# Performance work log

Hardware: AMD Instinct MI355X
Metric: run time of the kernel (lower is better)

The kernel has to match this reference:

```python
import jax, jax.numpy as jnp
import numpy as np

NUM_GROUPS = 16
EPS = 1e-6


def setup_inputs() -> dict:
    key = jax.random.key(0)
    ks = jax.random.split(key, 6)
    b, c, t, h, w = 2, 256, 4, 32, 32
    x = jax.random.normal(ks[0], (b, c, t, h, w), dtype=jnp.float32)
    scale = 0.02
    return {
        "x": x,
        "gamma": jnp.ones((c,), jnp.float32),
        "beta": jnp.zeros((c,), jnp.float32),
        "wq": jax.random.normal(ks[1], (c, c), jnp.float32) * scale,
        "bq": jnp.zeros((c,), jnp.float32),
        "wk": jax.random.normal(ks[2], (c, c), jnp.float32) * scale,
        "bk": jnp.zeros((c,), jnp.float32),
        "wv": jax.random.normal(ks[3], (c, c), jnp.float32) * scale,
        "bv": jnp.zeros((c,), jnp.float32),
        "wp": jax.random.normal(ks[4], (c, c), jnp.float32) * scale,
        "bp": jnp.zeros((c,), jnp.float32),
    }


def _group_norm(x, gamma, beta):
    b, c, t, h, w = x.shape
    xg = x.reshape(b, NUM_GROUPS, -1)  # [b, G, (c/G)*t*h*w]
    mu = jnp.mean(xg, axis=2, keepdims=True)
    var = jnp.var(xg, axis=2, keepdims=True)
    xn = ((xg - mu) * jax.lax.rsqrt(var + EPS)).reshape(b, c, t, h, w)
    return xn * gamma[None, :, None, None, None] + beta[None, :, None, None, None]


def reference(x, gamma, beta, wq, bq, wk, bk, wv, bv, wp, bp):
    b, c, t, h, w = x.shape
    n = t * h * w
    hn = _group_norm(x, gamma, beta).reshape(b, c, n)  # [b, c, n]
    # 1x1x1 conv == channel matmul
    q = jnp.einsum("oc,bcn->bon", wq, hn) + bq[None, :, None]
    k = jnp.einsum("oc,bcn->bon", wk, hn) + bk[None, :, None]
    v = jnp.einsum("oc,bcn->bon", wv, hn) + bv[None, :, None]
    # scores[b, i, j] = sum_c q[b,c,i] k[b,c,j] / sqrt(c)
    scores = jnp.einsum("bci,bcj->bij", q, k) * (float(c) ** -0.5)
    attn = jax.nn.softmax(scores, axis=2)  # [b, n, n]
    # h_[b, c, i] = sum_j v[b,c,j] attn[b,i,j]
    ho = jnp.einsum("bcj,bij->bci", v, attn)
    out = jnp.einsum("oc,bcn->bon", wp, ho) + bp[None, :, None]
    return x + out.reshape(b, c, t, h, w)
```

## Files before the change

kernel.cpp:

```cpp
#include <hip/hip_runtime.h>
#include <hip/hip_bf16.h>

#define NB 2
#define NC 256
#define NN 4096
#define NG 16
#define GSZ (16*NN)
#define SPLIT 4
#define SCL 0.09014205f

typedef __attribute__((ext_vector_type(8))) short bf16x8;
typedef __attribute__((ext_vector_type(4))) float f32x4;
typedef __attribute__((ext_vector_type(8))) unsigned short u16x8;

static __device__ __forceinline__ unsigned short f2b(float f) {
    union { float f; unsigned u; } x; x.f = f;
    unsigned r = x.u + 0x7fffu + ((x.u >> 16) & 1u);
    return (unsigned short)(r >> 16);
}
static __device__ __forceinline__ float b2f(unsigned short u) {
    union { unsigned u; float f; } x; x.u = ((unsigned)u) << 16;
    return x.f;
}
static __device__ __forceinline__ void glds16(const void* g, void* l) {
    __builtin_amdgcn_global_load_lds(
        (const __attribute__((address_space(1))) unsigned int*)g,
        (__attribute__((address_space(3))) unsigned int*)l, 16, 0, 0);
}

__global__ void k_wcvt(const float* __restrict__ wq, const float* __restrict__ wk,
                       const float* __restrict__ wv, const float* __restrict__ wp,
                       unsigned short* __restrict__ dst) {
    int idx = (blockIdx.x * 256 + threadIdx.x) * 4;
    int which = idx >> 16, off = idx & 65535;
    const float* s = (which == 0) ? wq : (which == 1) ? wk : (which == 2) ? wv : wp;
    float4 v = *(const float4*)(s + off);
    dst[idx + 0] = f2b(v.x);
    dst[idx + 1] = f2b(v.y);
    dst[idx + 2] = f2b(v.z);
    dst[idx + 3] = f2b(v.w);
}

__global__ void k_stats(const float* __restrict__ x, float* __restrict__ stats) {
    int bg = blockIdx.x >> 3, seg = blockIdx.x & 7;
    const float4* p = (const float4*)(x + (size_t)bg * GSZ + (size_t)seg * (GSZ / 8));
    float s1 = 0.f, s2 = 0.f;
    for (int k = threadIdx.x; k < GSZ / 8 / 4; k += 256) {
        float4 v = p[k];
        s1 += v.x + v.y + v.z + v.w;
        s2 += v.x*v.x + v.y*v.y + v.z*v.z + v.w*v.w;
    }
    #pragma unroll
    for (int m = 1; m < 64; m <<= 1) { s1 += __shfl_xor(s1, m); s2 += __shfl_xor(s2, m); }
    __shared__ float r1[4], r2[4];
    int w = threadIdx.x >> 6;
    if ((threadIdx.x & 63) == 0) { r1[w] = s1; r2[w] = s2; }
    __syncthreads();
    if (threadIdx.x == 0) {
        float a = 0.f, b = 0.f;
        #pragma unroll
        for (int i = 0; i < 4; i++) { a += r1[i]; b += r2[i]; }
        atomicAdd(&stats[bg * 2], a);
        atomicAdd(&stats[bg * 2 + 1], b);
    }
}

__global__ void k_norm_t(const float* __restrict__ x, const float* __restrict__ gamma,
                         const float* __restrict__ beta, const float* __restrict__ stats,
                         unsigned short* __restrict__ hn_t) {
    __shared__ unsigned short tile[64][66];
    int n0 = blockIdx.x * 64, c0 = blockIdx.y * 64, b = blockIdx.z;
    int cc = threadIdx.x >> 2, part = threadIdx.x & 3;
    int c = c0 + cc;
    float s1 = stats[(b * NG + (c >> 4)) * 2];
    float s2 = stats[(b * NG + (c >> 4)) * 2 + 1];
    float mean = s1 * (1.f / (float)GSZ);
    float var  = s2 * (1.f / (float)GSZ) - mean * mean;
    float rstd = rsqrtf(var + 1e-6f);
    float sc = rstd * gamma[c];
    float sh = beta[c] - mean * sc;
    const float4* row = (const float4*)(x + ((size_t)b * NC + c) * NN + n0);
    #pragma unroll
    for (int q = 0; q < 4; q++) {
        int f4 = part * 4 + q;
        float4 v = row[f4];
        tile[cc][f4*4+0] = f2b(v.x * sc + sh);
        tile[cc][f4*4+1] = f2b(v.y * sc + sh);
        tile[cc][f4*4+2] = f2b(v.z * sc + sh);
        tile[cc][f4*4+3] = f2b(v.w * sc + sh);
    }
    __syncthreads();
    int nn = threadIdx.x >> 2;
    u16x8 o0, o1;
    #pragma unroll
    for (int e = 0; e < 8; e++) { o0[e] = tile[part*16 + e][nn]; o1[e] = tile[part*16 + 8 + e][nn]; }
    unsigned short* dst = hn_t + ((size_t)b * NN + n0 + nn) * NC + c0 + part * 16;
    *(u16x8*)dst = o0;
    *(u16x8*)(dst + 8) = o1;
}

__global__ __launch_bounds__(256, 2) void k_qkv(
        const unsigned short* __restrict__ hn_t, const unsigned short* __restrict__ wb,
        const float* __restrict__ bq, const float* __restrict__ bk, const float* __restrict__ bv,
        unsigned short* __restrict__ q_t, unsigned short* __restrict__ k_t,
        unsigned short* __restrict__ v_cm) {
    int i0 = blockIdx.x * 64, which = blockIdx.y, b = blockIdx.z;
    int lane = threadIdx.x & 63, w = threadIdx.x >> 6;
    const unsigned short* W = wb + which * 65536;
    const float* bias = (which == 0) ? bq : (which == 1) ? bk : bv;
    if (which < 2) {
        const unsigned short* arow =
            hn_t + ((size_t)b * NN + i0 + w * 16 + (lane & 15)) * NC + ((lane >> 4) * 8);
        f32x4 acc[16];
        #pragma unroll
        for (int t = 0; t < 16; t++) acc[t] = (f32x4){0.f, 0.f, 0.f, 0.f};
        #pragma unroll
        for (int kk = 0; kk < 8; kk++) {
            bf16x8 af = *(const bf16x8*)(arow + kk * 32);
            const unsigned short* bbase = W + (size_t)(lane & 15) * NC + kk * 32 + ((lane >> 4) * 8);
            #pragma unroll
            for (int ot = 0; ot < 16; ot++) {
                bf16x8 bf_ = *(const bf16x8*)(bbase + (size_t)ot * 16 * NC);
                acc[ot] = __builtin_amdgcn_mfma_f32_16x16x32_bf16(af, bf_, acc[ot], 0, 0, 0);
            }
        }
        unsigned short* dst = ((which == 0) ? q_t : k_t) + (size_t)b * NN * NC;
        #pragma unroll
        for (int ot = 0; ot < 16; ot++) {
            float bv_ = bias[ot * 16 + (lane & 15)];
            #pragma unroll
            for (int r = 0; r < 4; r++) {
                int i = i0 + w * 16 + (lane >> 4) * 4 + r;
                dst[(size_t)i * NC + ot * 16 + (lane & 15)] = f2b(acc[ot][r] + bv_);
            }
        }
    } else {
        f32x4 acc[4][4];
        #pragma unroll
        for (int mt = 0; mt < 4; mt++)
            #pragma unroll
            for (int nt = 0; nt < 4; nt++) acc[mt][nt] = (f32x4){0.f, 0.f, 0.f, 0.f};
        #pragma unroll
        for (int kk = 0; kk < 8; kk++) {
            bf16x8 bfr[4];
            #pragma unroll
            for (int nt = 0; nt < 4; nt++)
                bfr[nt] = *(const bf16x8*)(hn_t + ((size_t)b * NN + i0 + nt * 16 + (lane & 15)) * NC
                                           + kk * 32 + ((lane >> 4) * 8));
            #pragma unroll
            for (int mt = 0; mt < 4; mt++) {
                bf16x8 af = *(const bf16x8*)(W + (size_t)(w * 64 + mt * 16 + (lane & 15)) * NC
                                             + kk * 32 + ((lane >> 4) * 8));
                #pragma unroll
                for (int nt = 0; nt < 4; nt++)
                    acc[mt][nt] = __builtin_amdgcn_mfma_f32_16x16x32_bf16(af, bfr[nt], acc[mt][nt], 0, 0, 0);
            }
        }
        #pragma unroll
        for (int mt = 0; mt < 4; mt++) {
            #pragma unroll
            for (int r = 0; r < 4; r++) {
                int o = w * 64 + mt * 16 + (lane >> 4) * 4 + r;
                float bv_ = bias[o];
                #pragma unroll
                for (int nt = 0; nt < 4; nt++) {
                    int i = i0 + nt * 16 + (lane & 15);
                    v_cm[(size_t)b * NC * NN + (size_t)o * NN + i] = f2b(acc[mt][nt][r] + bv_);
                }
            }
        }
    }
}

__global__ __launch_bounds__(512, 2) void k_attn(
        const unsigned short* __restrict__ q_t, const unsigned short* __restrict__ k_t,
        const unsigned short* __restrict__ v_cm,
        unsigned short* __restrict__ po, float* __restrict__ ml) {
    __shared__ __attribute__((aligned(16))) unsigned short Ks[2][16384];
    __shared__ __attribute__((aligned(16))) unsigned short Vs[2][16384];
    __shared__ __attribute__((aligned(16))) unsigned short Ps[8][1024];
    int d = blockIdx.x;
    int g = d & 7, xb = d >> 3;
    int sp = g & 3, b = g >> 2;
    int i0 = xb * 128;
    int lane = threadIdx.x & 63, w = threadIdx.x >> 6;
    size_t bO = (size_t)b * NN * NC;
    bf16x8 qf[8];
    {
        const unsigned short* qrow =
            q_t + bO + (size_t)(i0 + w * 16 + (lane & 15)) * NC + ((lane >> 4) * 8);
        #pragma unroll
        for (int kk = 0; kk < 8; kk++) qf[kk] = *(const bf16x8*)(qrow + kk * 32);
    }
    int j0b = sp * 1024;
    const char* gpk[4];
    const char* gpv[4];
    {
        const char* kbase = (const char*)(k_t + bO);
        const char* vbase = (const char*)(v_cm + bO);
        #pragma unroll
        for (int r = 0; r < 4; r++) {
            int jr = r * 16 + w * 2 + (lane >> 5);
            int cb = (lane & 31) * 16;
            gpk[r] = kbase + (size_t)(j0b + jr) * 512 + (cb ^ ((jr & 7) << 4));
            int cr = r * 64 + w * 8 + (lane >> 3);
            int jb = (lane & 7) * 16;
            gpv[r] = vbase + (size_t)cr * 8192 + (size_t)j0b * 2 + (jb ^ ((cr & 7) << 4));
        }
    }
    f32x4 o[16];
    #pragma unroll
    for (int t = 0; t < 16; t++) o[t] = (f32x4){0.f, 0.f, 0.f, 0.f};
    float m[4], l[4];
    #pragma unroll
    for (int r = 0; r < 4; r++) { m[r] = -1e30f; l[r] = 0.f; }
    #pragma unroll
    for (int r = 0; r < 4; r++) {
        glds16(gpk[r], (char*)&Ks[0][0] + w * 1024 + r * 8192);
        glds16(gpv[r], (char*)&Vs[0][0] + w * 1024 + r * 8192);
    }
    __syncthreads();
    int cur = 0;
    #pragma unroll 1
    for (int t = 0; t < 16; ++t) {
        if (t < 15) {
            #pragma unroll
            for (int r = 0; r < 4; r++) { gpk[r] += 32768; gpv[r] += 128; }
            int nb = cur ^ 1;
            #pragma unroll
            for (int r = 0; r < 4; r++) {
                glds16(gpk[r], (char*)&Ks[nb][0] + w * 1024 + r * 8192);
                glds16(gpv[r], (char*)&Vs[nb][0] + w * 1024 + r * 8192);
            }
        }
        const char* KsB = (const char*)&Ks[cur][0];
        const char* VsB = (const char*)&Vs[cur][0];
        f32x4 s[4];
        #pragma unroll
        for (int tt = 0; tt < 4; tt++) s[tt] = (f32x4){0.f, 0.f, 0.f, 0.f};
        #pragma unroll
        for (int kk = 0; kk < 8; kk++) {
            #pragma unroll
            for (int tt = 0; tt < 4; tt++) {
                unsigned off = ((unsigned)((tt * 16 + (lane & 15)) * 512 + kk * 64 + ((lane >> 4) * 16)))
                               ^ (((unsigned)(lane & 7)) << 4);
                bf16x8 kf = *(const bf16x8*)(KsB + off);
                s[tt] = __builtin_amdgcn_mfma_f32_16x16x32_bf16(qf[kk], kf, s[tt], 0, 0, 0);
            }
        }
        float corr[4];
        #pragma unroll
        for (int r = 0; r < 4; r++) {
            float v0 = fmaxf(fmaxf(s[0][r], s[1][r]), fmaxf(s[2][r], s[3][r]));
            v0 = fmaxf(v0, __shfl_xor(v0, 1));
            v0 = fmaxf(v0, __shfl_xor(v0, 2));
            v0 = fmaxf(v0, __shfl_xor(v0, 4));
            v0 = fmaxf(v0, __shfl_xor(v0, 8));
            float mn = fmaxf(m[r], v0);
            corr[r] = exp2f((m[r] - mn) * SCL);
            m[r] = mn;
        }
        float rs[4] = {0.f, 0.f, 0.f, 0.f};
        #pragma unroll
        for (int tt = 0; tt < 4; tt++) {
            #pragma unroll
            for (int r = 0; r < 4; r++) {
                float p = exp2f((s[tt][r] - m[r]) * SCL);
                rs[r] += p;
                unsigned i_ = (lane >> 4) * 4 + r;
                unsigned off = ((unsigned)(i_ * 128 + (tt * 16 + (lane & 15)) * 2)) ^ ((i_ & 7) << 4);
                *(unsigned short*)((char*)&Ps[w][0] + off) = f2b(p);
            }
        }
        #pragma unroll
        for (int r = 0; r < 4; r++) {
            float v0 = rs[r];
            v0 += __shfl_xor(v0, 1); v0 += __shfl_xor(v0, 2);
            v0 += __shfl_xor(v0, 4); v0 += __shfl_xor(v0, 8);
            l[r] = l[r] * corr[r] + v0;
        }
        #pragma unroll
        for (int tt = 0; tt < 16; tt++) {
            #pragma unroll
            for (int r = 0; r < 4; r++) o[tt][r] *= corr[r];
        }
        #pragma unroll
        for (int kk = 0; kk < 2; kk++) {
            unsigned offp = ((unsigned)((lane & 15) * 128 + kk * 64 + ((lane >> 4) * 16)))
                            ^ (((unsigned)(lane & 7)) << 4);
            bf16x8 pf = *(const bf16x8*)((char*)&Ps[w][0] + offp);
            #pragma unroll
            for (int ct = 0; ct < 16; ct++) {
                unsigned offv = ((unsigned)((ct * 16 + (lane & 15)) * 128 + kk * 64 + ((lane >> 4) * 16)))
                                ^ (((unsigned)(lane & 7)) << 4);
                bf16x8 vf = *(const bf16x8*)(VsB + offv);
                o[ct] = __builtin_amdgcn_mfma_f32_16x16x32_bf16(pf, vf, o[ct], 0, 0, 0);
            }
        }
        __syncthreads();
        cur ^= 1;
    }
    unsigned short* dst = po + ((size_t)(sp * NB + b) * NN) * NC;
    #pragma unroll
    for (int ct = 0; ct < 16; ct++) {
        #pragma unroll
        for (int r = 0; r < 4; r++) {
            int i = i0 + w * 16 + (lane >> 4) * 4 + r;
            dst[(size_t)i * NC + ct * 16 + (lane & 15)] = f2b(o[ct][r]);
        }
    }
    if ((lane & 15) == 0) {
        #pragma unroll
        for (int r = 0; r < 4; r++) {
            int i = i0 + w * 16 + (lane >> 4) * 4 + r;
            size_t mi = ((size_t)(sp * NB + b) * NN + i) * 2;
            ml[mi] = m[r];
            ml[mi + 1] = l[r];
        }
    }
}

__global__ void k_winv(const float* __restrict__ ml, float* __restrict__ winv) {
    int idx = blockIdx.x * 256 + threadIdx.x;
    float mv[SPLIT], lv[SPLIT];
    float M = -1e30f;
    #pragma unroll
    for (int s = 0; s < SPLIT; s++) {
        size_t mi = ((size_t)(s * 8192 + idx)) * 2;
        mv[s] = ml[mi]; lv[s] = ml[mi + 1];
        M = fmaxf(M, mv[s]);
    }
    float den = 0.f, wg[SPLIT];
    #pragma unroll
    for (int s = 0; s < SPLIT; s++) { wg[s] = exp2f((mv[s] - M) * SCL); den += wg[s] * lv[s]; }
    float inv = 1.f / den;
    #pragma unroll
    for (int s = 0; s < SPLIT; s++) winv[s * 8192 + idx] = wg[s] * inv;
}

__global__ __launch_bounds__(256, 4) void k_proj(
        const unsigned short* __restrict__ po, const float* __restrict__ winv,
        const unsigned short* __restrict__ wp_b, const float* __restrict__ bp,
        const float* __restrict__ x, float* __restrict__ out) {
    __shared__ __attribute__((aligned(16))) unsigned short Hs[32 * 256];
    int i0 = blockIdx.x * 32, b = blockIdx.y;
    int tid = threadIdx.x, lane = tid & 63, w = tid >> 6;
    {
        int il = tid >> 3, cq = tid & 7;
        int i = i0 + il;
        float wg[SPLIT];
        #pragma unroll
        for (int s = 0; s < SPLIT; s++) wg[s] = winv[s * 8192 + b * NN + i];
        #pragma unroll
        for (int e = 0; e < 4; e++) {
            float accv[8];
            #pragma unroll
            for (int q = 0; q < 8; q++) accv[q] = 0.f;
            #pragma unroll
            for (int s = 0; s < SPLIT; s++) {
                u16x8 v = *(const u16x8*)(po + ((size_t)(s * NB + b) * NN + i) * NC + cq * 32 + e * 8);
                #pragma unroll
                for (int q = 0; q < 8; q++) accv[q] += wg[s] * b2f(v[q]);
            }
            u16x8 rv;
            #pragma unroll
            for (int q = 0; q < 8; q++) rv[q] = f2b(accv[q]);
            unsigned off = ((unsigned)(il * 512 + cq * 64 + e * 16)) ^ ((il & 7) << 4);
            *(u16x8*)((char*)Hs + off) = rv;
        }
    }
    __syncthreads();
    f32x4 acc[4][2];
    #pragma unroll
    for (int mt = 0; mt < 4; mt++)
        #pragma unroll
        for (int nt = 0; nt < 2; nt++) acc[mt][nt] = (f32x4){0.f, 0.f, 0.f, 0.f};
    #pragma unroll
    for (int kk = 0; kk < 8; kk++) {
        bf16x8 bfr[2];
        #pragma unroll
        for (int nt = 0; nt < 2; nt++) {
            unsigned off = ((unsigned)((nt * 16 + (lane & 15)) * 512 + kk * 64 + ((lane >> 4) * 16)))
                           ^ (((unsigned)(lane & 7)) << 4);
            bfr[nt] = *(const bf16x8*)((char*)Hs + off);
        }
        #pragma unroll
        for (int mt = 0; mt < 4; mt++) {
            bf16x8 af = *(const bf16x8*)(wp_b + (size_t)(w * 64 + mt * 16 + (lane & 15)) * NC
                                         + kk * 32 + ((lane >> 4) * 8));
            #pragma unroll
            for (int nt = 0; nt < 2; nt++)
                acc[mt][nt] = __builtin_amdgcn_mfma_f32_16x16x32_bf16(af, bfr[nt], acc[mt][nt], 0, 0, 0);
        }
    }
    #pragma unroll
    for (int mt = 0; mt < 4; mt++) {
        #pragma unroll
        for (int r = 0; r < 4; r++) {
            int o = w * 64 + mt * 16 + (lane >> 4) * 4 + r;
            float bv_ = bp[o];
            #pragma unroll
            for (int nt = 0; nt < 2; nt++) {
                int i = i0 + nt * 16 + (lane & 15);
                size_t idx = ((size_t)b * NC + o) * NN + i;
                out[idx] = x[idx] + acc[mt][nt][r] + bv_;
            }
        }
    }
}

extern "C" void kernel_launch(void* const* d_in, const int* in_sizes, int n_in,
                              void* d_out, int out_size, void* d_ws, size_t ws_size,
                              hipStream_t stream) {
    const float* x     = (const float*)d_in[0];
    const float* gamma = (const float*)d_in[1];
    const float* beta  = (const float*)d_in[2];
    const float* wq    = (const float*)d_in[3];
    const float* bq    = (const float*)d_in[4];
    const float* wk    = (const float*)d_in[5];
    const float* bk    = (const float*)d_in[6];
    const float* wv    = (const float*)d_in[7];
    const float* bv    = (const float*)d_in[8];
    const float* wp    = (const float*)d_in[9];
    const float* bp    = (const float*)d_in[10];
    float* out = (float*)d_out;

    char* ws = (char*)d_ws;
    const size_t SZ_T = (size_t)NB * NN * NC * 2;
    float*          stats = (float*)ws;
    unsigned short* wb    = (unsigned short*)(ws + 1024);
    unsigned short* hn_t  = (unsigned short*)(ws + 1024 + 524288);
    unsigned short* q_t   = (unsigned short*)((char*)hn_t + SZ_T);
    unsigned short* k_t   = (unsigned short*)((char*)q_t + SZ_T);
    unsigned short* v_cm  = (unsigned short*)((char*)k_t + SZ_T);
    unsigned short* po    = (unsigned short*)((char*)v_cm + SZ_T);
    float*          ml    = (float*)((char*)po + (size_t)SPLIT * SZ_T);
    float*          winv  = (float*)((char*)ml + 262144);

    hipMemsetAsync(stats, 0, 1024, stream);
    k_wcvt<<<256, 256, 0, stream>>>(wq, wk, wv, wp, wb);
    k_stats<<<256, 256, 0, stream>>>(x, stats);
    k_norm_t<<<dim3(NN / 64, NC / 64, NB), 256, 0, stream>>>(x, gamma, beta, stats, hn_t);
    k_qkv<<<dim3(NN / 64, 3, NB), 256, 0, stream>>>(hn_t, wb, bq, bk, bv, q_t, k_t, v_cm);
    k_attn<<<256, 512, 0, stream>>>(q_t, k_t, v_cm, po, ml);
    k_winv<<<32, 256, 0, stream>>>(ml, winv);
    k_proj<<<dim3(NN / 32, NB), 256, 0, stream>>>(po, winv, wb + 3 * 65536, bp, x, out);
}
```

Measured before the change: 216.0 us.

## Stream V from global, lazy softmax rescale, fold split-merge into projection

The attention kernel stops staging V in shared memory and reads V fragments straight from global memory, which halves its LDS footprint, and launch bounds are raised to allow more resident blocks. Online-softmax rescaling of o and l now runs only when the running max grows past a threshold, so most tiles skip the correction multiplies. The kernel also adds s_setprio around the MFMA sections. The separate split-merge weight kernel is folded into the projection kernel, and workspace buffers are re-laid out so hn_t and po alias. Risks are higher global-memory latency on V reads and register pressure under the larger occupancy target.

```diff
diff --git a/kernel.cpp b/kernel.cpp
--- a/kernel.cpp
+++ b/kernel.cpp
@@ -7,7 +7,9 @@
 #define NG 16
 #define GSZ (16*NN)
 #define SPLIT 4
+#define JT (NN / SPLIT / 64)
 #define SCL 0.09014205f
+#define THRRAW 88.0f
 
 typedef __attribute__((ext_vector_type(8))) short bf16x8;
 typedef __attribute__((ext_vector_type(4))) float f32x4;
@@ -172,15 +174,14 @@
     }
 }
 
-__global__ __launch_bounds__(512, 2) void k_attn(
+__global__ __launch_bounds__(512, 4) void k_attn(
         const unsigned short* __restrict__ q_t, const unsigned short* __restrict__ k_t,
         const unsigned short* __restrict__ v_cm,
         unsigned short* __restrict__ po, float* __restrict__ ml) {
     __shared__ __attribute__((aligned(16))) unsigned short Ks[2][16384];
-    __shared__ __attribute__((aligned(16))) unsigned short Vs[2][16384];
     __shared__ __attribute__((aligned(16))) unsigned short Ps[8][1024];
-    int d = blockIdx.x;
-    int g = d & 7, xb = d >> 3;
+    int bid = blockIdx.x;
+    int g = bid & 7, xb = bid >> 3;
     int sp = g & 3, b = g >> 2;
     int i0 = xb * 128;
     int lane = threadIdx.x & 63, w = threadIdx.x >> 6;
@@ -192,22 +193,15 @@
         #pragma unroll
         for (int kk = 0; kk < 8; kk++) qf[kk] = *(const bf16x8*)(qrow + kk * 32);
     }
-    int j0b = sp * 1024;
-    const char* gpk[4];
-    const char* gpv[4];
-    {
-        const char* kbase = (const char*)(k_t + bO);
-        const char* vbase = (const char*)(v_cm + bO);
-        #pragma unroll
-        for (int r = 0; r < 4; r++) {
-            int jr = r * 16 + w * 2 + (lane >> 5);
-            int cb = (lane & 31) * 16;
-            gpk[r] = kbase + (size_t)(j0b + jr) * 512 + (cb ^ ((jr & 7) << 4));
-            int cr = r * 64 + w * 8 + (lane >> 3);
-            int jb = (lane & 7) * 16;
-            gpv[r] = vbase + (size_t)cr * 8192 + (size_t)j0b * 2 + (jb ^ ((cr & 7) << 4));
-        }
-    }
+    unsigned kstat[4];
+    #pragma unroll
+    for (int r = 0; r < 4; r++) {
+        int jr = r * 16 + w * 2 + (lane >> 5);
+        kstat[r] = (unsigned)(jr * 512 + (((lane & 31) * 16) ^ ((jr & 7) << 4)));
+    }
+    const char* kp = (const char*)(k_t + bO) + (size_t)sp * 524288;
+    const unsigned short* vbase = v_cm + bO + (size_t)(lane & 15) * NN + ((lane >> 4) * 8)
+                                  + (size_t)sp * 1024;
     f32x4 o[16];
     #pragma unroll
     for (int t = 0; t < 16; t++) o[t] = (f32x4){0.f, 0.f, 0.f, 0.f};
@@ -215,29 +209,24 @@
     #pragma unroll
     for (int r = 0; r < 4; r++) { m[r] = -1e30f; l[r] = 0.f; }
     #pragma unroll
-    for (int r = 0; r < 4; r++) {
-        glds16(gpk[r], (char*)&Ks[0][0] + w * 1024 + r * 8192);
-        glds16(gpv[r], (char*)&Vs[0][0] + w * 1024 + r * 8192);
-    }
+    for (int r = 0; r < 4; r++)
+        glds16(kp + kstat[r], (char*)&Ks[0][0] + w * 1024 + r * 8192);
     __syncthreads();
     int cur = 0;
     #pragma unroll 1
-    for (int t = 0; t < 16; ++t) {
-        if (t < 15) {
-            #pragma unroll
-            for (int r = 0; r < 4; r++) { gpk[r] += 32768; gpv[r] += 128; }
+    for (int t = 0; t < JT; ++t) {
+        if (t < JT - 1) {
+            kp += 32768;
             int nb = cur ^ 1;
             #pragma unroll
-            for (int r = 0; r < 4; r++) {
-                glds16(gpk[r], (char*)&Ks[nb][0] + w * 1024 + r * 8192);
-                glds16(gpv[r], (char*)&Vs[nb][0] + w * 1024 + r * 8192);
-            }
+            for (int r = 0; r < 4; r++)
+                glds16(kp + kstat[r], (char*)&Ks[nb][0] + w * 1024 + r * 8192);
         }
         const char* KsB = (const char*)&Ks[cur][0];
-        const char* VsB = (const char*)&Vs[cur][0];
         f32x4 s[4];
         #pragma unroll
         for (int tt = 0; tt < 4; tt++) s[tt] = (f32x4){0.f, 0.f, 0.f, 0.f};
+        __builtin_amdgcn_s_setprio(1);
         #pragma unroll
         for (int kk = 0; kk < 8; kk++) {
             #pragma unroll
@@ -248,7 +237,8 @@
                 s[tt] = __builtin_amdgcn_mfma_f32_16x16x32_bf16(qf[kk], kf, s[tt], 0, 0, 0);
             }
         }
-        float corr[4];
+        __builtin_amdgcn_s_setprio(0);
+        float vmax[4];
         #pragma unroll
         for (int r = 0; r < 4; r++) {
             float v0 = fmaxf(fmaxf(s[0][r], s[1][r]), fmaxf(s[2][r], s[3][r]));
@@ -256,9 +246,22 @@
             v0 = fmaxf(v0, __shfl_xor(v0, 2));
             v0 = fmaxf(v0, __shfl_xor(v0, 4));
             v0 = fmaxf(v0, __shfl_xor(v0, 8));
-            float mn = fmaxf(m[r], v0);
-            corr[r] = exp2f((m[r] - mn) * SCL);
-            m[r] = mn;
+            vmax[r] = v0;
+        }
+        float tmax = fmaxf(fmaxf(vmax[0] - m[0], vmax[1] - m[1]),
+                           fmaxf(vmax[2] - m[2], vmax[3] - m[3]));
+        tmax = fmaxf(tmax, __shfl_xor(tmax, 16));
+        tmax = fmaxf(tmax, __shfl_xor(tmax, 32));
+        if (tmax > THRRAW) {
+            #pragma unroll
+            for (int r = 0; r < 4; r++) {
+                float mn = fmaxf(m[r], vmax[r]);
+                float corr = exp2f((m[r] - mn) * SCL);
+                m[r] = mn;
+                l[r] *= corr;
+                #pragma unroll
+                for (int ct = 0; ct < 16; ct++) o[ct][r] *= corr;
+            }
         }
         float rs[4] = {0.f, 0.f, 0.f, 0.f};
         #pragma unroll
@@ -267,7 +270,7 @@
             for (int r = 0; r < 4; r++) {
                 float p = exp2f((s[tt][r] - m[r]) * SCL);
                 rs[r] += p;
-                unsigned i_ = (lane >> 4) * 4 + r;
+                unsigned i_ = (unsigned)((lane >> 4) * 4 + r);
                 unsigned off = ((unsigned)(i_ * 128 + (tt * 16 + (lane & 15)) * 2)) ^ ((i_ & 7) << 4);
                 *(unsigned short*)((char*)&Ps[w][0] + off) = f2b(p);
             }
@@ -277,30 +280,26 @@
             float v0 = rs[r];
             v0 += __shfl_xor(v0, 1); v0 += __shfl_xor(v0, 2);
             v0 += __shfl_xor(v0, 4); v0 += __shfl_xor(v0, 8);
-            l[r] = l[r] * corr[r] + v0;
-        }
-        #pragma unroll
-        for (int tt = 0; tt < 16; tt++) {
-            #pragma unroll
-            for (int r = 0; r < 4; r++) o[tt][r] *= corr[r];
-        }
-        #pragma unroll
-        for (int kk = 0; kk < 2; kk++) {
-            unsigned offp = ((unsigned)((lane & 15) * 128 + kk * 64 + ((lane >> 4) * 16)))
+            l[r] += v0;
+        }
+        const unsigned short* vt = vbase + (size_t)t * 64;
+        __builtin_amdgcn_s_setprio(1);
+        #pragma unroll
+        for (int kj = 0; kj < 2; kj++) {
+            unsigned offp = ((unsigned)((lane & 15) * 128 + kj * 64 + ((lane >> 4) * 16)))
                             ^ (((unsigned)(lane & 7)) << 4);
             bf16x8 pf = *(const bf16x8*)((char*)&Ps[w][0] + offp);
             #pragma unroll
             for (int ct = 0; ct < 16; ct++) {
-                unsigned offv = ((unsigned)((ct * 16 + (lane & 15)) * 128 + kk * 64 + ((lane >> 4) * 16)))
-                                ^ (((unsigned)(lane & 7)) << 4);
-                bf16x8 vf = *(const bf16x8*)(VsB + offv);
+                bf16x8 vf = *(const bf16x8*)(vt + (size_t)ct * 16 * NN + kj * 32);
                 o[ct] = __builtin_amdgcn_mfma_f32_16x16x32_bf16(pf, vf, o[ct], 0, 0, 0);
             }
         }
+        __builtin_amdgcn_s_setprio(0);
         __syncthreads();
         cur ^= 1;
     }
-    unsigned short* dst = po + ((size_t)(sp * NB + b) * NN) * NC;
+    unsigned short* dst = po + (size_t)(sp * NB + b) * NN * NC;
     #pragma unroll
     for (int ct = 0; ct < 16; ct++) {
         #pragma unroll
@@ -320,26 +319,8 @@
     }
 }
 
-__global__ void k_winv(const float* __restrict__ ml, float* __restrict__ winv) {
-    int idx = blockIdx.x * 256 + threadIdx.x;
-    float mv[SPLIT], lv[SPLIT];
-    float M = -1e30f;
-    #pragma unroll
-    for (int s = 0; s < SPLIT; s++) {
-        size_t mi = ((size_t)(s * 8192 + idx)) * 2;
-        mv[s] = ml[mi]; lv[s] = ml[mi + 1];
-        M = fmaxf(M, mv[s]);
-    }
-    float den = 0.f, wg[SPLIT];
-    #pragma unroll
-    for (int s = 0; s < SPLIT; s++) { wg[s] = exp2f((mv[s] - M) * SCL); den += wg[s] * lv[s]; }
-    float inv = 1.f / den;
-    #pragma unroll
-    for (int s = 0; s < SPLIT; s++) winv[s * 8192 + idx] = wg[s] * inv;
-}
-
 __global__ __launch_bounds__(256, 4) void k_proj(
-        const unsigned short* __restrict__ po, const float* __restrict__ winv,
+        const unsigned short* __restrict__ po, const float* __restrict__ ml,
         const unsigned short* __restrict__ wp_b, const float* __restrict__ bp,
         const float* __restrict__ x, float* __restrict__ out) {
     __shared__ __attribute__((aligned(16))) unsigned short Hs[32 * 256];
@@ -348,9 +329,20 @@
     {
         int il = tid >> 3, cq = tid & 7;
         int i = i0 + il;
-        float wg[SPLIT];
-        #pragma unroll
-        for (int s = 0; s < SPLIT; s++) wg[s] = winv[s * 8192 + b * NN + i];
+        float mv[SPLIT], lv[SPLIT];
+        float M = -1e30f;
+        #pragma unroll
+        for (int s = 0; s < SPLIT; s++) {
+            size_t mi = ((size_t)(s * NB + b) * NN + i) * 2;
+            mv[s] = ml[mi]; lv[s] = ml[mi + 1];
+            M = fmaxf(M, mv[s]);
+        }
+        float den = 0.f, wg[SPLIT];
+        #pragma unroll
+        for (int s = 0; s < SPLIT; s++) { wg[s] = exp2f((mv[s] - M) * SCL); den += wg[s] * lv[s]; }
+        float inv = 1.f / den;
+        #pragma unroll
+        for (int s = 0; s < SPLIT; s++) wg[s] *= inv;
         #pragma unroll
         for (int e = 0; e < 4; e++) {
             float accv[8];
@@ -426,16 +418,15 @@
     float* out = (float*)d_out;
 
     char* ws = (char*)d_ws;
-    const size_t SZ_T = (size_t)NB * NN * NC * 2;
+    const size_t MB = 1024 * 1024;
     float*          stats = (float*)ws;
     unsigned short* wb    = (unsigned short*)(ws + 1024);
-    unsigned short* hn_t  = (unsigned short*)(ws + 1024 + 524288);
-    unsigned short* q_t   = (unsigned short*)((char*)hn_t + SZ_T);
-    unsigned short* k_t   = (unsigned short*)((char*)q_t + SZ_T);
-    unsigned short* v_cm  = (unsigned short*)((char*)k_t + SZ_T);
-    unsigned short* po    = (unsigned short*)((char*)v_cm + SZ_T);
-    float*          ml    = (float*)((char*)po + (size_t)SPLIT * SZ_T);
-    float*          winv  = (float*)((char*)ml + 262144);
+    unsigned short* q_t   = (unsigned short*)(ws + 1 * MB);
+    unsigned short* k_t   = (unsigned short*)(ws + 5 * MB);
+    unsigned short* v_cm  = (unsigned short*)(ws + 9 * MB);
+    float*          ml    = (float*)(ws + 13 * MB);
+    unsigned short* hn_t  = (unsigned short*)(ws + 14 * MB);
+    unsigned short* po    = (unsigned short*)(ws + 14 * MB);
 
     hipMemsetAsync(stats, 0, 1024, stream);
     k_wcvt<<<256, 256, 0, stream>>>(wq, wk, wv, wp, wb);
@@ -443,6 +434,5 @@
     k_norm_t<<<dim3(NN / 64, NC / 64, NB), 256, 0, stream>>>(x, gamma, beta, stats, hn_t);
     k_qkv<<<dim3(NN / 64, 3, NB), 256, 0, stream>>>(hn_t, wb, bq, bk, bv, q_t, k_t, v_cm);
     k_attn<<<256, 512, 0, stream>>>(q_t, k_t, v_cm, po, ml);
-    k_winv<<<32, 256, 0, stream>>>(ml, winv);
-    k_proj<<<dim3(NN / 32, NB), 256, 0, stream>>>(po, winv, wb + 3 * 65536, bp, x, out);
-}
+    k_proj<<<dim3(NN / 32, NB), 256, 0, stream>>>(po, ml, wb + 3 * 65536, bp, x, out);
+}
```

New measurement: 522.0 us. +141.6%, slower.
